# Kernel tuning notes

Measured on AMD Instinct MI355X. Metric: run time of the kernel, lower is better.

The kernel has to match this reference:

```python
import jax, jax.numpy as jnp
import numpy as np

N, E, F, H, C = 100000, 1600000, 128, 128, 16
NEG_SLOPE = 0.01  # torch F.leaky_relu default


def setup_inputs() -> dict:
    key = jax.random.key(0)
    ks = jax.random.split(key, 32)
    inp = {
        "x": jax.random.normal(ks[0], (N, F), jnp.float32),
        "edge_index": jax.random.randint(ks[1], (2, E), 0, N, jnp.int32),
        "edge_weight": jax.random.uniform(ks[2], (E,), jnp.float32),
    }
    def w(k, fan_in, fan_out):
        s = 1.0 / np.sqrt(fan_in)
        return jax.random.uniform(k, (fan_in, fan_out), jnp.float32, -s, s)
    # cell 0: pre 128->128, arma 128->128, sage 128->128
    inp["pre_w0"] = w(ks[3], F, H); inp["pre_b0"] = jnp.zeros((H,), jnp.float32)
    inp["arma_w0"] = w(ks[4], H, H); inp["arma_v0"] = w(ks[5], H, H); inp["arma_b0"] = jnp.zeros((H,), jnp.float32)
    inp["sage_wl0"] = w(ks[6], H, H); inp["sage_bl0"] = jnp.zeros((H,), jnp.float32); inp["sage_wr0"] = w(ks[7], H, H)
    # cell 1: pre 256->128 (cell0 outputs 2H)
    inp["pre_w1"] = w(ks[8], 2 * H, H); inp["pre_b1"] = jnp.zeros((H,), jnp.float32)
    inp["arma_w1"] = w(ks[9], H, H); inp["arma_v1"] = w(ks[10], H, H); inp["arma_b1"] = jnp.zeros((H,), jnp.float32)
    inp["sage_wl1"] = w(ks[11], H, H); inp["sage_bl1"] = jnp.zeros((H,), jnp.float32); inp["sage_wr1"] = w(ks[12], H, H)
    inp["cls_w"] = w(ks[13], 2 * H, C); inp["cls_b"] = jnp.zeros((C,), jnp.float32)
    return inp


def _cell(h, row, col, norm, ew, cnt, n, arma_w, arma_v, arma_b, sage_wl, sage_bl, sage_wr):
    # ARMAConv (num_stacks=1, num_layers=1): relu(A_hat (h W) + h V + b), A_hat = sym-norm adj (no self loops)
    t = h @ arma_w
    agg = jax.ops.segment_sum(norm[:, None] * t[row], col, num_segments=n)
    h1 = jax.nn.leaky_relu(jax.nn.relu(agg + h @ arma_v + arma_b), NEG_SLOPE)
    # SAGEConv (mean aggr of edge-weighted messages): lin_l(mean_j w_ij h_j) + lin_r(h_i)
    s = jax.ops.segment_sum(ew[:, None] * h[row], col, num_segments=n)
    h2 = jax.nn.leaky_relu((s / cnt[:, None]) @ sage_wl + sage_bl + h @ sage_wr, NEG_SLOPE)
    return jax.nn.elu(jnp.concatenate([h1, h2], axis=1))


def reference(x, edge_index, edge_weight,
              pre_w0, pre_b0, arma_w0, arma_v0, arma_b0, sage_wl0, sage_bl0, sage_wr0,
              pre_w1, pre_b1, arma_w1, arma_v1, arma_b1, sage_wl1, sage_bl1, sage_wr1,
              cls_w, cls_b):
    n = x.shape[0]
    row, col = edge_index[0], edge_index[1]  # messages flow row -> col
    # gcn_norm without self loops (ARMAConv)
    deg = jax.ops.segment_sum(edge_weight, col, num_segments=n)
    dinv = jnp.where(deg > 0, 1.0 / jnp.sqrt(jnp.where(deg > 0, deg, 1.0)), 0.0)
    norm = dinv[row] * edge_weight * dinv[col]
    # scatter_mean denominator (edge counts, clamped to 1)
    cnt = jnp.maximum(jax.ops.segment_sum(jnp.ones_like(edge_weight), col, num_segments=n), 1.0)
    h = x  # eval mode: input dropout is identity
    for p in [(pre_w0, pre_b0, arma_w0, arma_v0, arma_b0, sage_wl0, sage_bl0, sage_wr0),
              (pre_w1, pre_b1, arma_w1, arma_v1, arma_b1, sage_wl1, sage_bl1, sage_wr1)]:
        pw, pb = p[0], p[1]
        h = _cell(h @ pw + pb, row, col, norm, edge_weight, cnt, n, *p[2:])
    logits = h @ cls_w + cls_b
    return jax.nn.log_softmax(logits, axis=-1)
```

## Files before the change

kernel.cpp:

```cpp
#include <hip/hip_runtime.h>
#include <hip/hip_bf16.h>
#include <hip/hip_fp16.h>

typedef __bf16 bf16x8 __attribute__((ext_vector_type(8)));
typedef float f32x4 __attribute__((ext_vector_type(4)));
typedef unsigned short ushort_t;
typedef unsigned int uint_t;

#if defined(__has_builtin)
#if __has_builtin(__builtin_amdgcn_global_load_lds)
#define HAS_GLL 1
#endif
#endif

__device__ inline float blo(uint_t v) { return __uint_as_float(v << 16); }
__device__ inline float bhi(uint_t v) { return __uint_as_float(v & 0xffff0000u); }
__device__ inline ushort_t f2b(float f) {
  uint_t u = __float_as_uint(f);
  uint_t r = (u + 0x7fffu + ((u >> 16) & 1u)) >> 16;
  return (ushort_t)r;
}
__device__ inline uint_t pk2(float a, float b) {
  return (uint_t)f2b(a) | ((uint_t)f2b(b) << 16);
}


__global__ __launch_bounds__(256) void bcount_k(const int* __restrict__ col,
                                                int* __restrict__ bcnt, int E, int NB) {
  __shared__ int h[256];
  int t = threadIdx.x;
  h[t] = 0;
  __syncthreads();
  int e0 = blockIdx.x * 8192;
#pragma unroll
  for (int j = 0; j < 32; ++j) {
    int e = e0 + j * 256 + t;
    if (e < E) atomicAdd(&h[col[e] >> 9], 1);
  }
  __syncthreads();
  if (t < NB && h[t] > 0) atomicAdd(&bcnt[t], h[t]);
}

__global__ __launch_bounds__(256) void bscan_k(const int* __restrict__ bcnt,
                                               int* __restrict__ bbase, int* __restrict__ cursor,
                                               int* __restrict__ offs, int NB, int N, int E) {
  __shared__ int sd[256];
  int t = threadIdx.x;
  int v = (t < NB) ? bcnt[t] : 0;
  int acc = v;
  sd[t] = v; __syncthreads();
  for (int off = 1; off < 256; off <<= 1) {
    int x = (t >= off) ? sd[t - off] : 0;
    __syncthreads();
    acc += x; sd[t] = acc;
    __syncthreads();
  }
  if (t < NB) { bbase[t] = acc - v; cursor[t] = acc - v; }
  if (t == 0) { bbase[NB] = E; offs[N] = E; }
}

__global__ __launch_bounds__(512) void bscatter_k(
    const int* __restrict__ row, const int* __restrict__ col, const float* __restrict__ ew,
    int* __restrict__ cursor, uint2* __restrict__ eout, int E, int NB) {
  __shared__ int h[256];
  __shared__ int lofs[256];
  __shared__ int lcur[256];
  __shared__ int gbase[256];
  __shared__ int sc[256];
  __shared__ uint2 stage[8192];
  __shared__ int addr[8192];
  int t = threadIdx.x;
  int e0 = blockIdx.x * 8192;
  int cnt = min(8192, E - e0);
  if (t < 256) h[t] = 0;
  __syncthreads();
#pragma unroll
  for (int j = 0; j < 16; ++j) {
    int e = e0 + j * 512 + t;
    if (e < E) atomicAdd(&h[col[e] >> 9], 1);
  }
  __syncthreads();
  int s = (t < 256) ? h[t] : 0;
  int acc = s;
  if (t < 256) sc[t] = s;
  __syncthreads();
  for (int off = 1; off < 256; off <<= 1) {
    int x = (t < 256 && t >= off) ? sc[t - off] : 0;
    __syncthreads();
    if (t < 256) { acc += x; sc[t] = acc; }
    __syncthreads();
  }
  if (t < NB && s > 0) gbase[t] = atomicAdd(&cursor[t], s);
  if (t < 256) { lofs[t] = acc - s; lcur[t] = acc - s; }
  __syncthreads();
#pragma unroll
  for (int j = 0; j < 16; ++j) {
    int e = e0 + j * 512 + t;
    if (e < E) {
      int c = col[e];
      int bk = c >> 9;
      int p = atomicAdd(&lcur[bk], 1);
      uint2 v;
      v.x = ((uint_t)(c & 511) << 17) | (uint_t)row[e];
      v.y = __float_as_uint(ew[e]);
      stage[p] = v;
      addr[p] = gbase[bk] + (p - lofs[bk]);
    }
  }
  __syncthreads();
  for (int i = t; i < cnt; i += 512) eout[addr[i]] = stage[i];
}

__global__ __launch_bounds__(512) void bsort_k(
    const uint2* __restrict__ ein, const int* __restrict__ bbase,
    int* __restrict__ offs, float* __restrict__ dinv, float* __restrict__ cinv,
    uint2* __restrict__ eout, int N) {
  __shared__ int h[512];
  __shared__ int lcur[512];
  __shared__ float degs[512];
  __shared__ int sd[512];
  int t = threadIdx.x, b = blockIdx.x;
  int base = bbase[b], end = bbase[b + 1];
  int cnt = end - base;
  int node0 = b << 9;
  h[t] = 0;
  degs[t] = 0.f;
  __syncthreads();
  for (int i = t; i < cnt; i += 512) {
    uint2 v = ein[base + i];
    int lc = v.x >> 17;
    atomicAdd(&h[lc], 1);
    atomicAdd(&degs[lc], __uint_as_float(v.y));
  }
  __syncthreads();
  int s = h[t];
  int acc = s;
  sd[t] = s; __syncthreads();
  for (int off = 1; off < 512; off <<= 1) {
    int x = (t >= off) ? sd[t - off] : 0;
    __syncthreads();
    acc += x; sd[t] = acc;
    __syncthreads();
  }
  int excl = acc - s;
  lcur[t] = excl;
  int node = node0 + t;
  if (node < N) {
    offs[node] = base + excl;
    float d = degs[t];
    dinv[node] = d > 0.f ? rsqrtf(d) : 0.f;
    cinv[node] = 1.0f / fmaxf((float)s, 1.f);
  }
  __syncthreads();
  for (int i = t; i < cnt; i += 512) {
    uint2 v = ein[base + i];
    int lc = v.x >> 17;
    int p = atomicAdd(&lcur[lc], 1);
    uint2 o;
    o.x = v.x & 0x1FFFF;
    o.y = v.y;
    eout[base + p] = o;
  }
}

__global__ void edgew_k(uint2* __restrict__ sedge, const float* __restrict__ dinv, int E) {
  int e = blockIdx.x * blockDim.x + threadIdx.x;
  if (e < E) {
    uint2 v = sedge[e];
    float ew = __uint_as_float(v.y);
    float wA = dinv[v.x] * ew;
    uint_t lo = (uint_t)__half_as_ushort(__float2half_rn(wA));
    uint_t hi = (uint_t)__half_as_ushort(__float2half_rn(ew));
    sedge[e].y = lo | (hi << 16);
  }
}

struct WP { const float* p[12]; };
__global__ void wtp_k(WP wp, ushort_t* __restrict__ wt) {
  int b = blockIdx.x;
  int t = threadIdx.x;
  if (b < 11) {
    const float* W = wp.p[b];
    ushort_t* T = wt + (size_t)b * 128 * 128;
    for (int i = 0; i < 64; ++i) {
      int lin = i * 256 + t;
      int k = lin >> 7, c = lin & 127;
      T[c * 128 + k] = f2b(W[lin]);
    }
  } else {
    const float* W = wp.p[11];
    ushort_t* T = wt + (size_t)11 * 128 * 128;
    for (int i = 0; i < 16; ++i) {
      int lin = i * 256 + t;
      int c = lin >> 8, k = lin & 255;
      T[lin] = f2b(W[k * 16 + c]);
    }
  }
}

__global__ __launch_bounds__(256) void agg_k(
    const uint_t* __restrict__ hp2, const uint2* __restrict__ sedge,
    const float* __restrict__ dinv, const float* __restrict__ cinv,
    const int* __restrict__ offs,
    uint_t* __restrict__ outA, uint_t* __restrict__ outS, int n) {
  int wid = threadIdx.x >> 6;
  int lane = threadIdx.x & 63;
  int half = lane >> 5, li = lane & 31;
  int node = blockIdx.x * 8 + wid * 2 + half;
  if (node >= n) return;
  int s0 = offs[node], e0 = offs[node + 1];
  const char* hpb = (const char*)hp2;
  uint_t libase = (uint_t)(li << 3);
  float a0 = 0.f, a1 = 0.f, a2 = 0.f, a3 = 0.f;
  float m0 = 0.f, m1 = 0.f, m2 = 0.f, m3 = 0.f;
  for (int p = s0; p < e0; p += 8) {
    uint2 ed[8];
#pragma unroll
    for (int j = 0; j < 8; ++j) {
      int k = p + j;
      ed[j] = sedge[k < e0 ? k : s0];
    }
#pragma unroll
    for (int j = 0; j < 8; ++j) {
      bool ok = (p + j < e0);
      uint_t w = ok ? ed[j].y : 0u;
      uint_t vo = (ed[j].x << 8) | libase;
      uint2 v = *(const uint2*)(hpb + vo);
      float wA = __half2float(__ushort_as_half((ushort_t)(w & 0xffff)));
      float wS = __half2float(__ushort_as_half((ushort_t)(w >> 16)));
      float f0 = blo(v.x), f1 = bhi(v.x), f2 = blo(v.y), f3 = bhi(v.y);
      a0 += wA * f0; a1 += wA * f1; a2 += wA * f2; a3 += wA * f3;
      m0 += wS * f0; m1 += wS * f1; m2 += wS * f2; m3 += wS * f3;
    }
  }
  float dn = dinv[node], cn = cinv[node];
  uint2 oA, oS;
  oA.x = pk2(dn * a0, dn * a1); oA.y = pk2(dn * a2, dn * a3);
  oS.x = pk2(cn * m0, cn * m1); oS.y = pk2(cn * m2, cn * m3);
  *(uint2*)&outA[(size_t)node * 64 + li * 2] = oA;
  *(uint2*)&outS[(size_t)node * 64 + li * 2] = oS;
}

__device__ inline int swz(int r, int k) { return (r * 128 + k) ^ ((r & 7) << 3); }
__device__ inline int cswz(int r, int k) { return (r * 256 + k) ^ ((r & 7) << 3); }

__device__ inline void stage_tile(const ushort_t* __restrict__ A, ushort_t* lds,
                                  int rowBase, int wid, int lane) {
  int lr = lane >> 4, lchunk = lane & 15;
#ifdef HAS_GLL
#pragma unroll
  for (int i = 0; i < 8; ++i) {
    int r = wid * 32 + i * 4 + lr;
    int csrc = (lchunk ^ (r & 7)) << 4;
    const char* g = (const char*)A + (((size_t)(rowBase + r)) << 8) + csrc;
    char* l = (char*)lds + ((wid * 32 + i * 4) << 8);
    __builtin_amdgcn_global_load_lds((const __attribute__((address_space(1))) void*)g,
                                     (__attribute__((address_space(3))) void*)l, 16, 0, 0);
  }
#else
#pragma unroll
  for (int i = 0; i < 8; ++i) {
    int r = wid * 32 + i * 4 + lr;
    uint4 v = *(const uint4*)&A[((size_t)(rowBase + r)) * 128 + lchunk * 8];
    *(uint4*)&lds[swz(r, lchunk * 8)] = v;
  }
#endif
}

__device__ inline void stage_wait() {
#ifdef HAS_GLL
  asm volatile("s_waitcnt vmcnt(0)" ::: "memory");
#endif
}

__device__ inline bf16x8 ldw(const ushort_t* __restrict__ Wt, int wc, int nn, int k, int lane) {
  int c = wc * 64 + nn * 16 + (lane & 15);
  return *(const bf16x8*)&Wt[c * 128 + k * 32 + (lane >> 4) * 8];
}

__device__ inline bf16x8 lda(const ushort_t* lds, int wr, int m, int k, int lane) {
  return *(const bf16x8*)&lds[swz(wr * 64 + m * 16 + (lane & 15), k * 32 + (lane >> 4) * 8)];
}

template <int ACT>
__device__ inline void epilogue(f32x4 (&acc)[4][4], const float* __restrict__ bias,
                                ushort_t* __restrict__ out, int rowBase, int wr, int wc,
                                int lane, int nrows) {
#pragma unroll
  for (int m = 0; m < 4; ++m) {
    int gr0 = rowBase + wr * 64 + m * 16 + (lane >> 4) * 4;
#pragma unroll
    for (int nn = 0; nn < 4; ++nn) {
      int gc = wc * 64 + nn * 16 + (lane & 15);
      float bv = bias[gc];
#pragma unroll
      for (int j = 0; j < 4; ++j) {
        int gr = gr0 + j;
        if (gr < nrows) {
          float v = acc[m][nn][j] + bv;
          if (ACT == 1) v = fmaxf(v, 0.f);
          if (ACT == 2) v = v > 0.f ? v : (__expf(0.01f * v) - 1.f);
          out[(size_t)gr * 128 + gc] = f2b(v);
        }
      }
    }
  }
}

__global__ __launch_bounds__(256, 2) void pre0_k(
    const float* __restrict__ Xf, const ushort_t* __restrict__ Wt,
    const float* __restrict__ bias, ushort_t* __restrict__ out, int nrows) {
  __shared__ ushort_t As[128 * 128];
  int t = threadIdx.x, lane = t & 63, wid = t >> 6;
  int wr = wid >> 1, wc = wid & 1;
  int rowBase = blockIdx.x * 128;
#pragma unroll
  for (int i = 0; i < 16; ++i) {
    int f = t + i * 256;
    int r = f >> 5, q = f & 31;
    int gr = rowBase + r;
    float4 v = make_float4(0.f, 0.f, 0.f, 0.f);
    if (gr < nrows) v = *(const float4*)&Xf[(size_t)gr * 128 + q * 4];
    uint2 o;
    o.x = pk2(v.x, v.y);
    o.y = pk2(v.z, v.w);
    *(uint2*)&As[swz(r, q * 4)] = o;
  }
  __syncthreads();
  f32x4 acc[4][4] = {};
#pragma unroll
  for (int k = 0; k < 4; ++k) {
    bf16x8 af[4], wf[4];
#pragma unroll
    for (int m = 0; m < 4; ++m) af[m] = lda(As, wr, m, k, lane);
#pragma unroll
    for (int nn = 0; nn < 4; ++nn) wf[nn] = ldw(Wt, wc, nn, k, lane);
#pragma unroll
    for (int m = 0; m < 4; ++m)
#pragma unroll
      for (int nn = 0; nn < 4; ++nn)
        acc[m][nn] = __builtin_amdgcn_mfma_f32_16x16x32_bf16(af[m], wf[nn], acc[m][nn], 0, 0, 0);
  }
  epilogue<0>(acc, bias, out, rowBase, wr, wc, lane, nrows);
}

template <int TAIL>
__global__ __launch_bounds__(256, 2) void dualfused_k(
    const ushort_t* __restrict__ X, const ushort_t* __restrict__ Y,
    const ushort_t* __restrict__ H,
    const ushort_t* __restrict__ WX, const ushort_t* __restrict__ WXH,
    const ushort_t* __restrict__ WY, const ushort_t* __restrict__ WYH,
    const float* __restrict__ bX, const float* __restrict__ bY,
    const ushort_t* __restrict__ WZ1, const ushort_t* __restrict__ WZ2,
    const float* __restrict__ bZ,
    ushort_t* __restrict__ outH, float* __restrict__ outL, int nrows) {
  __shared__ ushort_t buf[2 * 128 * 128];
  ushort_t* Xs = buf;
  ushort_t* Hs = buf + 128 * 128;
  int t = threadIdx.x, lane = t & 63, wid = t >> 6;
  int wr = wid >> 1, wc = wid & 1;
  int rowBase = blockIdx.x * 128;

  stage_tile(X, Xs, rowBase, wid, lane);
  stage_tile(H, Hs, rowBase, wid, lane);
  stage_wait();
  __syncthreads();

  uint_t h1p[4][4][2];
  {
    f32x4 acc[4][4] = {};
#pragma unroll
    for (int k = 0; k < 4; ++k) {
      bf16x8 af[4], hf[4], wx[4], wh[4];
#pragma unroll
      for (int m = 0; m < 4; ++m) { af[m] = lda(Xs, wr, m, k, lane); hf[m] = lda(Hs, wr, m, k, lane); }
#pragma unroll
      for (int nn = 0; nn < 4; ++nn) { wx[nn] = ldw(WX, wc, nn, k, lane); wh[nn] = ldw(WXH, wc, nn, k, lane); }
#pragma unroll
      for (int m = 0; m < 4; ++m)
#pragma unroll
        for (int nn = 0; nn < 4; ++nn) {
          acc[m][nn] = __builtin_amdgcn_mfma_f32_16x16x32_bf16(af[m], wx[nn], acc[m][nn], 0, 0, 0);
          acc[m][nn] = __builtin_amdgcn_mfma_f32_16x16x32_bf16(hf[m], wh[nn], acc[m][nn], 0, 0, 0);
        }
    }
#pragma unroll
    for (int m = 0; m < 4; ++m)
#pragma unroll
      for (int nn = 0; nn < 4; ++nn) {
        float bv = bX[wc * 64 + nn * 16 + (lane & 15)];
        float v0 = fmaxf(acc[m][nn][0] + bv, 0.f);
        float v1 = fmaxf(acc[m][nn][1] + bv, 0.f);
        float v2 = fmaxf(acc[m][nn][2] + bv, 0.f);
        float v3 = fmaxf(acc[m][nn][3] + bv, 0.f);
        h1p[m][nn][0] = pk2(v0, v1);
        h1p[m][nn][1] = pk2(v2, v3);
      }
  }

  __syncthreads();
  stage_tile(Y, Xs, rowBase, wid, lane);
  stage_wait();
  __syncthreads();

  f32x4 acc2[4][4] = {};
#pragma unroll
  for (int k = 0; k < 4; ++k) {
    bf16x8 af[4], hf[4], wy[4], wh[4];
#pragma unroll
    for (int m = 0; m < 4; ++m) { af[m] = lda(Xs, wr, m, k, lane); hf[m] = lda(Hs, wr, m, k, lane); }
#pragma unroll
    for (int nn = 0; nn < 4; ++nn) { wy[nn] = ldw(WY, wc, nn, k, lane); wh[nn] = ldw(WYH, wc, nn, k, lane); }
#pragma unroll
    for (int m = 0; m < 4; ++m)
#pragma unroll
      for (int nn = 0; nn < 4; ++nn) {
        acc2[m][nn] = __builtin_amdgcn_mfma_f32_16x16x32_bf16(af[m], wy[nn], acc2[m][nn], 0, 0, 0);
        acc2[m][nn] = __builtin_amdgcn_mfma_f32_16x16x32_bf16(hf[m], wh[nn], acc2[m][nn], 0, 0, 0);
      }
  }

  __syncthreads();

#pragma unroll
  for (int m = 0; m < 4; ++m) {
    int r0 = wr * 64 + m * 16 + (lane >> 4) * 4;
#pragma unroll
    for (int nn = 0; nn < 4; ++nn) {
      int c = wc * 64 + nn * 16 + (lane & 15);
      float bv = bY[c];
#pragma unroll
      for (int j = 0; j < 4; ++j) {
        int r = r0 + j;
        ushort_t h1v = (ushort_t)((h1p[m][nn][j >> 1] >> ((j & 1) * 16)) & 0xffff);
        buf[cswz(r, c)] = h1v;
        float v = acc2[m][nn][j] + bv;
        v = v > 0.f ? v : (__expf(0.01f * v) - 1.f);
        buf[cswz(r, 128 + c)] = f2b(v);
      }
    }
  }
  __syncthreads();

  if (TAIL == 0) {
    f32x4 acc3[4][4] = {};
#pragma unroll
    for (int kk = 0; kk < 8; ++kk) {
      const ushort_t* WZ = (kk < 4) ? WZ1 : WZ2;
      int kl = kk & 3;
      bf16x8 af[4], wf[4];
#pragma unroll
      for (int m = 0; m < 4; ++m) {
        int r = wr * 64 + m * 16 + (lane & 15);
        af[m] = *(const bf16x8*)&buf[cswz(r, kk * 32 + (lane >> 4) * 8)];
      }
#pragma unroll
      for (int nn = 0; nn < 4; ++nn) wf[nn] = ldw(WZ, wc, nn, kl, lane);
#pragma unroll
      for (int m = 0; m < 4; ++m)
#pragma unroll
        for (int nn = 0; nn < 4; ++nn)
          acc3[m][nn] = __builtin_amdgcn_mfma_f32_16x16x32_bf16(af[m], wf[nn], acc3[m][nn], 0, 0, 0);
    }
    epilogue<0>(acc3, bZ, outH, rowBase, wr, wc, lane, nrows);
  } else {
    f32x4 accc[2] = {};
#pragma unroll
    for (int kk = 0; kk < 8; ++kk) {
      bf16x8 bfr = *(const bf16x8*)&WZ1[(lane & 15) * 256 + kk * 32 + (lane >> 4) * 8];
#pragma unroll
      for (int mm = 0; mm < 2; ++mm) {
        int r = wid * 32 + mm * 16 + (lane & 15);
        bf16x8 af = *(const bf16x8*)&buf[cswz(r, kk * 32 + (lane >> 4) * 8)];
        accc[mm] = __builtin_amdgcn_mfma_f32_16x16x32_bf16(af, bfr, accc[mm], 0, 0, 0);
      }
    }
    float bc = bZ[lane & 15];
#pragma unroll
    for (int mm = 0; mm < 2; ++mm) {
#pragma unroll
      for (int j = 0; j < 4; ++j) {
        float lg = accc[mm][j] + bc;
        float mx = lg;
        for (int d = 1; d < 16; d <<= 1) mx = fmaxf(mx, __shfl_xor(mx, d));
        float ex = __expf(lg - mx);
        float sum = ex;
        for (int d = 1; d < 16; d <<= 1) sum += __shfl_xor(sum, d);
        float r_ = (lg - mx) - logf(sum);
        int grow = rowBase + wid * 32 + mm * 16 + (lane >> 4) * 4 + j;
        if (grow < nrows) outL[grow * 16 + (lane & 15)] = r_;
      }
    }
  }
}


extern "C" void kernel_launch(void* const* d_in, const int* in_sizes, int n_in,
                              void* d_out, int out_size, void* d_ws, size_t ws_size,
                              hipStream_t stream) {
  const float* x        = (const float*)d_in[0];
  const int*   eidx     = (const int*)d_in[1];
  const float* ew       = (const float*)d_in[2];
  const float* pre_w0   = (const float*)d_in[3];
  const float* pre_b0   = (const float*)d_in[4];
  const float* arma_w0  = (const float*)d_in[5];
  const float* arma_v0  = (const float*)d_in[6];
  const float* arma_b0  = (const float*)d_in[7];
  const float* sage_wl0 = (const float*)d_in[8];
  const float* sage_bl0 = (const float*)d_in[9];
  const float* sage_wr0 = (const float*)d_in[10];
  const float* pre_w1   = (const float*)d_in[11];
  const float* pre_b1   = (const float*)d_in[12];
  const float* arma_w1  = (const float*)d_in[13];
  const float* arma_v1  = (const float*)d_in[14];
  const float* arma_b1  = (const float*)d_in[15];
  const float* sage_wl1 = (const float*)d_in[16];
  const float* sage_bl1 = (const float*)d_in[17];
  const float* sage_wr1 = (const float*)d_in[18];
  const float* cls_w    = (const float*)d_in[19];
  const float* cls_b    = (const float*)d_in[20];

  const int N = in_sizes[0] / 128;
  const int E = in_sizes[2];
  const int N_pad = ((N + 127) / 128) * 128;
  const int NB = (N + 511) >> 9;
  const int* row = eidx;
  const int* col = eidx + E;

  char* p = (char*)d_ws;
  auto carve = [&](size_t bytes) { char* q = p; p += (bytes + 255) & ~(size_t)255; return q; };
  ushort_t* hp    = (ushort_t*)carve((size_t)N_pad * 128 * 2);
  ushort_t* bufA  = (ushort_t*)carve((size_t)N_pad * 128 * 2);
  ushort_t* bufS  = (ushort_t*)carve((size_t)N_pad * 128 * 2);
  ushort_t* wt    = (ushort_t*)carve(((size_t)11 * 128 * 128 + 16 * 256) * 2);
  uint2*  sedge  = (uint2*)carve((size_t)E * 8);
  uint2*  sedgeT = (uint2*)carve((size_t)E * 8);
  float*  dinv  = (float*)carve((size_t)N * 4);
  float*  cinv  = (float*)carve((size_t)N * 4);
  int*    offs  = (int*)carve((size_t)(N + 1) * 4);
  int*    bcnt  = (int*)carve((size_t)256 * 4);
  int*    bbase = (int*)carve((size_t)257 * 4);
  int*    cursor= (int*)carve((size_t)256 * 4);

  hipMemsetAsync(bcnt, 0, (size_t)256 * 4, stream);

  const int gE = (E + 8191) / 8192;
  bcount_k<<<gE, 256, 0, stream>>>(col, bcnt, E, NB);
  bscan_k<<<1, 256, 0, stream>>>(bcnt, bbase, cursor, offs, NB, N, E);
  bscatter_k<<<gE, 512, 0, stream>>>(row, col, ew, cursor, sedgeT, E, NB);
  bsort_k<<<NB, 512, 0, stream>>>(sedgeT, bbase, offs, dinv, cinv, sedge, N);
  edgew_k<<<(E + 255) / 256, 256, 0, stream>>>(sedge, dinv, E);

  WP wp;
  wp.p[0] = pre_w0;  wp.p[1] = arma_w0; wp.p[2] = arma_v0;
  wp.p[3] = sage_wl0; wp.p[4] = sage_wr0;
  wp.p[5] = pre_w1;  wp.p[6] = pre_w1 + 128 * 128;
  wp.p[7] = arma_w1; wp.p[8] = arma_v1;
  wp.p[9] = sage_wl1; wp.p[10] = sage_wr1;
  wp.p[11] = cls_w;
  wtp_k<<<12, 256, 0, stream>>>(wp, wt);

  const int gB = (N + 127) / 128;
  const int gA = (N + 7) / 8;
  auto WT = [&](int i) { return wt + (size_t)i * 128 * 128; };

  pre0_k<<<gB, 256, 0, stream>>>(x, WT(0), pre_b0, hp, N);
  agg_k<<<gA, 256, 0, stream>>>((const uint_t*)hp, sedge, dinv, cinv, offs, (uint_t*)bufA, (uint_t*)bufS, N);
  dualfused_k<0><<<gB, 256, 0, stream>>>(bufA, bufS, hp, WT(1), WT(2), WT(3), WT(4),
                                         arma_b0, sage_bl0, WT(5), WT(6), pre_b1,
                                         hp, nullptr, N);
  agg_k<<<gA, 256, 0, stream>>>((const uint_t*)hp, sedge, dinv, cinv, offs, (uint_t*)bufA, (uint_t*)bufS, N);
  dualfused_k<1><<<gB, 256, 0, stream>>>(bufA, bufS, hp, WT(7), WT(8), WT(9), WT(10),
                                         arma_b1, sage_bl1, WT(11), nullptr, cls_b,
                                         nullptr, (float*)d_out, N);
}
```

Before: 377.8 us.

## Process aggregation nodes in degree-sorted order to balance wavefront work

Bins nodes by in-degree (capped at 255) during the edge sort, then builds a node list grouped by degree with a histogram, scan and fill pass. The aggregation kernel reads its node id from this list, so the two half-waves in each wavefront handle nodes with similar edge counts. The aim is less divergence and idle lanes from unequal neighbour loops. In exchange it adds three small kernels and an extra indirection, and nodes are visited in a scattered order, which may hurt output-write locality.

Result: slower. 648.7 us (+71.7%).

```diff
diff --git a/kernel.cpp b/kernel.cpp
--- a/kernel.cpp
+++ b/kernel.cpp
@@ -114,7 +114,7 @@
 __global__ __launch_bounds__(512) void bsort_k(
     const uint2* __restrict__ ein, const int* __restrict__ bbase,
     int* __restrict__ offs, float* __restrict__ dinv, float* __restrict__ cinv,
-    uint2* __restrict__ eout, int N) {
+    int* __restrict__ dbin, uint2* __restrict__ eout, int N) {
   __shared__ int h[512];
   __shared__ int lcur[512];
   __shared__ float degs[512];
@@ -150,6 +150,7 @@
     float d = degs[t];
     dinv[node] = d > 0.f ? rsqrtf(d) : 0.f;
     cinv[node] = 1.0f / fmaxf((float)s, 1.f);
+    dbin[node] = min(s, 255);
   }
   __syncthreads();
   for (int i = t; i < cnt; i += 512) {
@@ -172,6 +173,48 @@
     uint_t lo = (uint_t)__half_as_ushort(__float2half_rn(wA));
     uint_t hi = (uint_t)__half_as_ushort(__float2half_rn(ew));
     sedge[e].y = lo | (hi << 16);
+  }
+}
+
+__global__ __launch_bounds__(256) void dhist_k(const int* __restrict__ dbin,
+                                               int* __restrict__ dh, int n) {
+  __shared__ int h[256];
+  int t = threadIdx.x;
+  h[t] = 0;
+  __syncthreads();
+  int base = blockIdx.x * 1024;
+#pragma unroll
+  for (int j = 0; j < 4; ++j) {
+    int i = base + j * 256 + t;
+    if (i < n) atomicAdd(&h[dbin[i]], 1);
+  }
+  __syncthreads();
+  if (h[t] > 0) atomicAdd(&dh[t], h[t]);
+}
+
+__global__ __launch_bounds__(256) void dscan_k(const int* __restrict__ dh,
+                                               int* __restrict__ dcur) {
+  __shared__ int sd[256];
+  int t = threadIdx.x;
+  int v = dh[t];
+  int acc = v;
+  sd[t] = v; __syncthreads();
+  for (int off = 1; off < 256; off <<= 1) {
+    int x = (t >= off) ? sd[t - off] : 0;
+    __syncthreads();
+    acc += x; sd[t] = acc;
+    __syncthreads();
+  }
+  dcur[t] = acc - v;
+}
+
+__global__ __launch_bounds__(256) void dfill_k(const int* __restrict__ dbin,
+                                               int* __restrict__ dcur,
+                                               int* __restrict__ nodelist, int n) {
+  int i = blockIdx.x * blockDim.x + threadIdx.x;
+  if (i < n) {
+    int pos = atomicAdd(&dcur[dbin[i]], 1);
+    nodelist[pos] = i;
   }
 }
 
@@ -201,13 +244,14 @@
 __global__ __launch_bounds__(256) void agg_k(
     const uint_t* __restrict__ hp2, const uint2* __restrict__ sedge,
     const float* __restrict__ dinv, const float* __restrict__ cinv,
-    const int* __restrict__ offs,
+    const int* __restrict__ offs, const int* __restrict__ nodelist,
     uint_t* __restrict__ outA, uint_t* __restrict__ outS, int n) {
   int wid = threadIdx.x >> 6;
   int lane = threadIdx.x & 63;
   int half = lane >> 5, li = lane & 31;
-  int node = blockIdx.x * 8 + wid * 2 + half;
-  if (node >= n) return;
+  int idx = blockIdx.x * 8 + wid * 2 + half;
+  if (idx >= n) return;
+  int node = nodelist[idx];
   int s0 = offs[node], e0 = offs[node + 1];
   const char* hpb = (const char*)hp2;
   uint_t libase = (uint_t)(li << 3);
@@ -538,18 +582,25 @@
   float*  dinv  = (float*)carve((size_t)N * 4);
   float*  cinv  = (float*)carve((size_t)N * 4);
   int*    offs  = (int*)carve((size_t)(N + 1) * 4);
+  int*    dbin  = (int*)carve((size_t)N * 4);
+  int*    nodelist = (int*)carve((size_t)N * 4);
   int*    bcnt  = (int*)carve((size_t)256 * 4);
+  int*    dh    = (int*)carve((size_t)256 * 4);
   int*    bbase = (int*)carve((size_t)257 * 4);
   int*    cursor= (int*)carve((size_t)256 * 4);
-
-  hipMemsetAsync(bcnt, 0, (size_t)256 * 4, stream);
+  int*    dcur  = (int*)carve((size_t)256 * 4);
+
+  hipMemsetAsync(bcnt, 0, (size_t)512 * 4, stream);
 
   const int gE = (E + 8191) / 8192;
   bcount_k<<<gE, 256, 0, stream>>>(col, bcnt, E, NB);
   bscan_k<<<1, 256, 0, stream>>>(bcnt, bbase, cursor, offs, NB, N, E);
   bscatter_k<<<gE, 512, 0, stream>>>(row, col, ew, cursor, sedgeT, E, NB);
-  bsort_k<<<NB, 512, 0, stream>>>(sedgeT, bbase, offs, dinv, cinv, sedge, N);
+  bsort_k<<<NB, 512, 0, stream>>>(sedgeT, bbase, offs, dinv, cinv, dbin, sedge, N);
   edgew_k<<<(E + 255) / 256, 256, 0, stream>>>(sedge, dinv, E);
+  dhist_k<<<(N + 1023) / 1024, 256, 0, stream>>>(dbin, dh, N);
+  dscan_k<<<1, 256, 0, stream>>>(dh, dcur);
+  dfill_k<<<(N + 255) / 256, 256, 0, stream>>>(dbin, dcur, nodelist, N);
 
   WP wp;
   wp.p[0] = pre_w0;  wp.p[1] = arma_w0; wp.p[2] = arma_v0;
@@ -565,11 +616,13 @@
   auto WT = [&](int i) { return wt + (size_t)i * 128 * 128; };
 
   pre0_k<<<gB, 256, 0, stream>>>(x, WT(0), pre_b0, hp, N);
-  agg_k<<<gA, 256, 0, stream>>>((const uint_t*)hp, sedge, dinv, cinv, offs, (uint_t*)bufA, (uint_t*)bufS, N);
+  agg_k<<<gA, 256, 0, stream>>>((const uint_t*)hp, sedge, dinv, cinv, offs, nodelist,
+                                (uint_t*)bufA, (uint_t*)bufS, N);
   dualfused_k<0><<<gB, 256, 0, stream>>>(bufA, bufS, hp, WT(1), WT(2), WT(3), WT(4),
                                          arma_b0, sage_bl0, WT(5), WT(6), pre_b1,
                                          hp, nullptr, N);
-  agg_k<<<gA, 256, 0, stream>>>((const uint_t*)hp, sedge, dinv, cinv, offs, (uint_t*)bufA, (uint_t*)bufS, N);
+  agg_k<<<gA, 256, 0, stream>>>((const uint_t*)hp, sedge, dinv, cinv, offs, nodelist,
+                                (uint_t*)bufA, (uint_t*)bufS, N);
   dualfused_k<1><<<gB, 256, 0, stream>>>(bufA, bufS, hp, WT(7), WT(8), WT(9), WT(10),
                                          arma_b1, sage_bl1, WT(11), nullptr, cls_b,
                                          nullptr, (float*)d_out, N);
```
